# Optimization experiments

Measured on AMD Instinct MI355X. Metric: run time of the kernel, lower is better.

Reference implementation:

```python
import jax, jax.numpy as jnp
import numpy as np

B, S, H, W = 16, 512, 768, 8


def _enumerate_spans(S, W):
    # same enumeration order as the torch triple loop: for i, for j in [i, min(i+W, S)-1]
    starts, widths = [], []
    for i in range(S):
        for w in range(1, min(W, S - i) + 1):
            starts.append(i)
            widths.append(w)
    return np.asarray(starts, np.int32), np.asarray(widths, np.int32)


def setup_inputs() -> dict:
    key = jax.random.key(0)
    k1, k2, k3 = jax.random.split(key, 3)
    embeddings = jax.random.normal(k1, (B, S, H), dtype=jnp.float32)
    w_lin = jax.random.normal(k2, (2 * H + 1, H), dtype=jnp.float32) * 0.02
    b_lin = jax.random.normal(k3, (H,), dtype=jnp.float32) * 0.02
    starts, widths = _enumerate_spans(S, W)
    return {
        "embeddings": embeddings,
        "w_lin": w_lin,
        "b_lin": b_lin,
        "span_starts": jnp.asarray(starts),
        "span_widths": jnp.asarray(widths),
    }


def reference(embeddings, w_lin, b_lin, span_starts, span_widths):
    Bb, Ss, Hh = embeddings.shape
    cls_emb = embeddings[:, 0, :]  # [B, H]

    # Sliding-window running max: pooled[k, b, i, :] = max(embeddings[b, i:i+k+1, :])
    neg = jnp.full((Bb, W - 1, Hh), -jnp.inf, embeddings.dtype)
    padded = jnp.concatenate([embeddings, neg], axis=1)  # [B, S+W-1, H]
    cm = embeddings
    pools = [cm]
    for k in range(1, W):
        cm = jnp.maximum(cm, padded[:, k:k + Ss, :])
        pools.append(cm)
    pooled = jnp.stack(pools, axis=0)  # [W, B, S, H]

    # Gather each span's max-pooled embedding: [N, B, H] -> [B, N, H]
    span_max = pooled[span_widths - 1, :, span_starts, :]
    span_max = jnp.transpose(span_max, (1, 0, 2))

    N = span_starts.shape[0]
    cls_b = jnp.broadcast_to(cls_emb[:, None, :], (Bb, N, Hh))
    width_f = jnp.broadcast_to(
        span_widths.astype(embeddings.dtype)[None, :, None], (Bb, N, 1))
    feats = jnp.concatenate([span_max, cls_b, width_f], axis=-1)  # [B, N, 2H+1]

    span_reps = jnp.einsum("bnf,fh->bnh", feats, w_lin) + b_lin
    token_inputs = cls_emb  # [B, H]
    return token_inputs, span_reps.reshape(Bb * N, Hh)
```

## Files before the change

### kernel.cpp

```cpp
#include <hip/hip_runtime.h>
#include <hip/hip_bf16.h>
#include <stdint.h>

#define AS1 __attribute__((address_space(1)))
#define AS3 __attribute__((address_space(3)))

typedef float  f32x4  __attribute__((ext_vector_type(4)));
typedef __bf16 bf16x8 __attribute__((ext_vector_type(8)));
typedef __bf16 bf16x4 __attribute__((ext_vector_type(4)));
typedef short  s16x8  __attribute__((ext_vector_type(8)));

static constexpr int Bc = 16, Sc = 512, Hc = 768, NSPAN = 4068;

__global__ __launch_bounds__(256)
void prep_w1t(const float* __restrict__ w_lin, unsigned short* __restrict__ w1t, int swz) {
  __shared__ __align__(16) unsigned short T[64][80];
  int bidk = blockIdx.x % 12, bidn = blockIdx.x / 12;
  int k0 = bidk * 64, n0 = bidn * 64;
  int tid = threadIdx.x;
#pragma unroll
  for (int p = 0; p < 16; ++p) {
    int idx = p * 256 + tid;
    int kl = idx >> 6, nl = idx & 63;
    float v = w_lin[(size_t)(k0 + kl) * Hc + (n0 + nl)];
    __bf16 bv = (__bf16)v;
    T[nl][kl] = __builtin_bit_cast(unsigned short, bv);
  }
  __syncthreads();
#pragma unroll
  for (int qq = 0; qq < 2; ++qq) {
    int q = qq * 256 + tid;
    int nl = q >> 3, cc = q & 7;
    int n = n0 + nl;
    s16x8 v = *(const s16x8*)(&T[nl][cc * 8]);
    size_t off;
    if (swz) {
      int q8 = (k0 >> 3) + cc;
      off = (size_t)n * 1536 + (size_t)(q8 >> 2) * 64 + (size_t)((q8 & 3) ^ (n & 3)) * 16;
    } else {
      off = (size_t)n * 1536 + (size_t)k0 * 2 + (size_t)cc * 16;
    }
    *(s16x8*)((char*)w1t + off) = v;
  }
}

__global__ __launch_bounds__(256)
void cls_proj_kernel(const float* __restrict__ emb, const float* __restrict__ w_lin,
                     const float* __restrict__ b_lin, float* __restrict__ out,
                     float* __restrict__ cls_proj) {
  __shared__ float cls_s[Hc];
  int b = blockIdx.x / 3, hc = blockIdx.x % 3;
  int tid = threadIdx.x;
  const float* cls = emb + (size_t)b * Sc * Hc;
  for (int i = tid; i < Hc; i += 256) cls_s[i] = cls[i];
  __syncthreads();
  int h = hc * 256 + tid;
  const float* wp = w_lin + (size_t)Hc * Hc + h;
  float p0 = 0, p1 = 0, p2 = 0, p3 = 0, p4 = 0, p5 = 0, p6 = 0, p7 = 0;
  for (int f = 0; f < Hc; f += 8) {
    p0 += cls_s[f + 0] * wp[(size_t)(f + 0) * Hc];
    p1 += cls_s[f + 1] * wp[(size_t)(f + 1) * Hc];
    p2 += cls_s[f + 2] * wp[(size_t)(f + 2) * Hc];
    p3 += cls_s[f + 3] * wp[(size_t)(f + 3) * Hc];
    p4 += cls_s[f + 4] * wp[(size_t)(f + 4) * Hc];
    p5 += cls_s[f + 5] * wp[(size_t)(f + 5) * Hc];
    p6 += cls_s[f + 6] * wp[(size_t)(f + 6) * Hc];
    p7 += cls_s[f + 7] * wp[(size_t)(f + 7) * Hc];
  }
  float acc = b_lin[h] + (((p0 + p1) + (p2 + p3)) + ((p4 + p5) + (p6 + p7)));
  cls_proj[b * Hc + h] = acc;
  out[b * Hc + h] = cls_s[h];
}

__global__ __launch_bounds__(256)
void build_a(const float* __restrict__ emb, unsigned short* __restrict__ a_ws) {
  int blk = blockIdx.x;
  int b = blk >> 6, sb = blk & 63;
  int tid = threadIdx.x;
  int si = tid >> 5, kc = tid & 31;
  int s = (sb << 3) + si;
  const char* embB = (const char*)(emb + (size_t)b * Sc * Hc);
  uint32_t roff[8];
#pragma unroll
  for (int t = 0; t < 8; ++t) {
    int r = s + t;
    if (r > 511) r = 511;
    roff[t] = (uint32_t)r * (Hc * 4);
  }
  char* obase = (char*)a_ws + (size_t)((b * 512 + s) * 8) * 1536;
#pragma unroll
  for (int j = 0; j < 3; ++j) {
    int q8 = kc + (j << 5);
    uint32_t srcoff = (uint32_t)q8 * 32;
    f32x4 c0, c1;
#pragma unroll
    for (int t = 0; t < 8; ++t) {
      f32x4 a0 = *(const f32x4*)(embB + roff[t] + srcoff);
      f32x4 a1 = *(const f32x4*)(embB + roff[t] + srcoff + 16);
      if (t == 0) { c0 = a0; c1 = a1; }
      else {
        c0[0] = fmaxf(c0[0], a0[0]); c0[1] = fmaxf(c0[1], a0[1]);
        c0[2] = fmaxf(c0[2], a0[2]); c0[3] = fmaxf(c0[3], a0[3]);
        c1[0] = fmaxf(c1[0], a1[0]); c1[1] = fmaxf(c1[1], a1[1]);
        c1[2] = fmaxf(c1[2], a1[2]); c1[3] = fmaxf(c1[3], a1[3]);
      }
      bf16x8 p;
      p[0] = (__bf16)c0[0]; p[1] = (__bf16)c0[1]; p[2] = (__bf16)c0[2]; p[3] = (__bf16)c0[3];
      p[4] = (__bf16)c1[0]; p[5] = (__bf16)c1[1]; p[6] = (__bf16)c1[2]; p[7] = (__bf16)c1[3];
      size_t doff = (size_t)t * 1536 + (size_t)(q8 >> 2) * 64 + (size_t)((q8 & 3) ^ (t & 3)) * 16;
      *(bf16x8*)(obase + doff) = p;
    }
  }
}

__global__ __launch_bounds__(512, 1)
void gemm_pipe(const unsigned short* __restrict__ a_ws, const unsigned short* __restrict__ w1t,
               const float* __restrict__ cls_proj, const float* __restrict__ w_lin,
               float* __restrict__ out) {
  extern __shared__ __align__(16) char ldsb[];

  int wg = blockIdx.x;
  int wgid = (wg & 7) * 96 + (wg >> 3);
  int tile_n = wgid % 3, tile_m = wgid / 3;
  int b = tile_m >> 4;
  int n0 = tile_n << 8;
  int tid = threadIdx.x;
  int wid = tid >> 6, lane = tid & 63;
  int wave_m = wid >> 2, wave_n = wid & 3;
  int lq = lane >> 4, lr = lane & 15;

  const char* aw = (const char*)a_ws + ((size_t)tile_m << 8) * 1536;
  const char* bw = (const char*)w1t + (size_t)n0 * 1536;
  int srow = tid >> 2, schunk = tid & 3;

  const float* w2p = w_lin + (size_t)(2 * Hc) * Hc;
  float cp[4], w2[4];
#pragma unroll
  for (int ni = 0; ni < 4; ++ni) {
    int h = n0 + (wave_n << 6) + (ni << 4) + lr;
    cp[ni] = cls_proj[b * Hc + h];
    w2[ni] = w2p[h];
  }

  f32x4 acc[8][4];
  f32x4 zer = {0.f, 0.f, 0.f, 0.f};
#pragma unroll
  for (int i = 0; i < 8; ++i)
#pragma unroll
    for (int j = 0; j < 4; ++j) acc[i][j] = zer;

  bf16x8 bfr[4];

#define SB __builtin_amdgcn_sched_barrier(0)

#define STAGE_A(kt) {                                                          \
    const char* s_ = aw + (size_t)srow * 1536 + (size_t)(kt) * 64 + (schunk << 4); \
    char* d_ = ldsb + (((kt) & 3) << 15) + (tid << 4);                         \
    __builtin_amdgcn_global_load_lds((const AS1 uint32_t*)s_, (AS3 uint32_t*)d_, 16, 0, 0); \
    __builtin_amdgcn_global_load_lds((const AS1 uint32_t*)(s_ + 128 * 1536), (AS3 uint32_t*)(d_ + 8192), 16, 0, 0); }

#define STAGE_B(kt) {                                                          \
    const char* s_ = bw + (size_t)srow * 1536 + (size_t)(kt) * 64 + (schunk << 4); \
    char* d_ = ldsb + (((kt) & 3) << 15) + 16384 + (tid << 4);                 \
    __builtin_amdgcn_global_load_lds((const AS1 uint32_t*)s_, (AS3 uint32_t*)d_, 16, 0, 0); \
    __builtin_amdgcn_global_load_lds((const AS1 uint32_t*)(s_ + 128 * 1536), (AS3 uint32_t*)(d_ + 8192), 16, 0, 0); }

#define PH0(kt, DOSTAGE) {                                                     \
    const char* Ab_ = ldsb + (((kt) & 3) << 15);                               \
    const char* Bb_ = Ab_ + 16384;                                             \
    _Pragma("unroll") for (int ni = 0; ni < 4; ++ni) {                         \
      int n = (wave_n << 6) + (ni << 4) + lr;                                  \
      bfr[ni] = *(const bf16x8*)(Bb_ + n * 64 + ((lq ^ (n & 3)) << 4));        \
    }                                                                          \
    bf16x8 af[4];                                                              \
    _Pragma("unroll") for (int mi = 0; mi < 4; ++mi) {                         \
      int m = (wave_m << 7) + (mi << 4) + lr;                                  \
      af[mi] = *(const bf16x8*)(Ab_ + m * 64 + ((lq ^ (m & 3)) << 4));         \
    }                                                                          \
    if (DOSTAGE) { STAGE_A((kt) + 3); }                                        \
    SB; __builtin_amdgcn_s_barrier(); SB;                                      \
    __builtin_amdgcn_s_setprio(1);                                             \
    _Pragma("unroll") for (int mi = 0; mi < 4; ++mi)                           \
      _Pragma("unroll") for (int ni = 0; ni < 4; ++ni)                         \
        acc[mi][ni] = __builtin_amdgcn_mfma_f32_16x16x32_bf16(af[mi], bfr[ni], acc[mi][ni], 0, 0, 0); \
    __builtin_amdgcn_s_setprio(0);                                             \
    __builtin_amdgcn_s_barrier(); }

#define PH1(kt, DOSTAGE, WAITASM) {                                            \
    const char* Ab_ = ldsb + (((kt) & 3) << 15);                               \
    bf16x8 af[4];                                                              \
    _Pragma("unroll") for (int mi = 0; mi < 4; ++mi) {                         \
      int m = (wave_m << 7) + 64 + (mi << 4) + lr;                             \
      af[mi] = *(const bf16x8*)(Ab_ + m * 64 + ((lq ^ (m & 3)) << 4));         \
    }                                                                          \
    if (DOSTAGE) { STAGE_B((kt) + 3); }                                        \
    SB; __builtin_amdgcn_s_barrier(); SB;                                      \
    __builtin_amdgcn_s_setprio(1);                                             \
    _Pragma("unroll") for (int mi = 0; mi < 4; ++mi)                           \
      _Pragma("unroll") for (int ni = 0; ni < 4; ++ni)                         \
        acc[4 + mi][ni] = __builtin_amdgcn_mfma_f32_16x16x32_bf16(af[mi], bfr[ni], acc[4 + mi][ni], 0, 0, 0); \
    __builtin_amdgcn_s_setprio(0);                                             \
    SB; asm volatile(WAITASM ::: "memory"); SB;                                \
    __builtin_amdgcn_s_barrier(); }

  STAGE_A(-3 + 3); STAGE_B(0);
  STAGE_A(1 - 3 + 3);
  {
    const char* s_ = aw + (size_t)srow * 1536 + (size_t)1 * 64 + (schunk << 4);
    char* d_ = ldsb + ((1 & 3) << 15) + (tid << 4);
    __builtin_amdgcn_global_load_lds((const AS1 uint32_t*)s_, (AS3 uint32_t*)d_, 16, 0, 0);
    __builtin_amdgcn_global_load_lds((const AS1 uint32_t*)(s_ + 128 * 1536), (AS3 uint32_t*)(d_ + 8192), 16, 0, 0);
  }
  STAGE_B(1);
  {
    const char* s_ = aw + (size_t)srow * 1536 + (size_t)2 * 64 + (schunk << 4);
    char* d_ = ldsb + ((2 & 3) << 15) + (tid << 4);
    __builtin_amdgcn_global_load_lds((const AS1 uint32_t*)s_, (AS3 uint32_t*)d_, 16, 0, 0);
    __builtin_amdgcn_global_load_lds((const AS1 uint32_t*)(s_ + 128 * 1536), (AS3 uint32_t*)(d_ + 8192), 16, 0, 0);
  }
  STAGE_B(2);
  SB; asm volatile("s_waitcnt vmcnt(8)" ::: "memory"); SB;
  __builtin_amdgcn_s_barrier(); SB;

  for (int kt = 0; kt < 21; ++kt) {
    PH0(kt, 1);
    PH1(kt, 1, "s_waitcnt vmcnt(8)");
  }
  PH0(21, 0); PH1(21, 0, "s_waitcnt vmcnt(4)");
  PH0(22, 0); PH1(22, 0, "s_waitcnt vmcnt(0)");
  PH0(23, 0); PH1(23, 0, "s_nop 0");

  float* outp = out + Bc * Hc;
  int swb = (tile_m & 15) << 8;
  int hbase = n0 + (wave_n << 6) + lr;
#pragma unroll
  for (int mi = 0; mi < 8; ++mi) {
#pragma unroll
    for (int j = 0; j < 4; ++j) {
      int m = (wave_m << 7) + (mi << 4) + (lq << 2) + j;
      int sw = swb + m;
      int s = sw >> 3, w = (sw & 7) + 1;
      if (s + w <= 512) {
        int nsp = (s <= 504) ? sw
                             : (NSPAN - (((512 - s) * (513 - s)) >> 1) + w - 1);
        float* rowp = outp + ((size_t)b * NSPAN + nsp) * Hc + hbase;
        float wf = (float)w;
#pragma unroll
        for (int ni = 0; ni < 4; ++ni)
          rowp[ni << 4] = acc[mi][ni][j] + cp[ni] + wf * w2[ni];
      }
    }
  }
}

__global__ __launch_bounds__(512, 2)
void span_gemm_fused(const float* __restrict__ emb, const unsigned short* __restrict__ w1t,
                     const float* __restrict__ cls_proj, const float* __restrict__ w_lin,
                     float* __restrict__ out) {
  __shared__ __align__(16) unsigned short Ald[2][256 * 64];
  int wg = blockIdx.x;
  int wgid = (wg & 7) * 96 + (wg >> 3);
  int tile_n = wgid % 3, tile_m = wgid / 3;
  int b = tile_m >> 4;
  int s0 = (tile_m & 15) << 5;
  int n0 = tile_n << 8;
  int tid = threadIdx.x;
  int wid = tid >> 6, lane = tid & 63;
  int wave_m = wid >> 2, wave_n = wid & 3;
  int lq = lane >> 4, lr = lane & 15;
  const char* embC = (const char*)(emb + (size_t)b * Sc * Hc);
  int bi = tid >> 4, bkq = tid & 15;
  uint32_t rowoff[8];
#pragma unroll
  for (int t = 0; t < 8; ++t) {
    int r = s0 + bi + t;
    if (r > 511) r = 511;
    rowoff[t] = (uint32_t)r * (Hc * 4) + bkq * 16;
  }
  int awbase = (bi << 10) + ((bkq & 1) << 3);
  const unsigned short* bb = w1t + (size_t)(n0 + (wave_n << 6) + lr) * Hc + (lq << 3);
  f32x4 acc[8][4];
  f32x4 zer = {0.f, 0.f, 0.f, 0.f};
#pragma unroll
  for (int i = 0; i < 8; ++i)
#pragma unroll
    for (int j = 0; j < 4; ++j) acc[i][j] = zer;
  f32x4 rv[8];
  f32x4 cm;
  bf16x8 bfrA[4], bfrB[4];
#define FLOAD_RV(koff) _Pragma("unroll") for (int t = 0; t < 8; ++t) rv[t] = *(const f32x4*)(embC + rowoff[t] + (koff));
#define FLOAD_BFR(dst, koff) _Pragma("unroll") for (int ni = 0; ni < 4; ++ni) dst[ni] = *(const bf16x8*)(const void*)(bb + (size_t)ni * 16 * Hc + (koff));
#define FBUILD_T(an, t) { \
    if ((t) == 0) cm = rv[0]; \
    else { cm[0] = fmaxf(cm[0], rv[t][0]); cm[1] = fmaxf(cm[1], rv[t][1]); cm[2] = fmaxf(cm[2], rv[t][2]); cm[3] = fmaxf(cm[3], rv[t][3]); } \
    bf16x4 p; p[0] = (__bf16)cm[0]; p[1] = (__bf16)cm[1]; p[2] = (__bf16)cm[2]; p[3] = (__bf16)cm[3]; \
    int off = awbase + ((t) << 7) + (((bkq >> 1) ^ (t)) << 4); \
    *(uint2*)((an) + off) = __builtin_bit_cast(uint2, p); }
#define FQUAD(ab, mh, kk, bfr) { \
    bf16x8 af[4]; int cf = ((kk) << 2) + lq; \
    _Pragma("unroll") for (int mi = 0; mi < 4; ++mi) { \
      int m = (wave_m << 7) + ((((mh) << 2) + mi) << 4) + lr; \
      af[mi] = *(const bf16x8*)((ab) + (m << 7) + ((cf ^ (m & 7)) << 4)); } \
    __builtin_amdgcn_s_setprio(1); \
    _Pragma("unroll") for (int mi = 0; mi < 4; ++mi) \
      _Pragma("unroll") for (int ni = 0; ni < 4; ++ni) \
        acc[((mh) << 2) + mi][ni] = __builtin_amdgcn_mfma_f32_16x16x32_bf16(af[mi], bfr[ni], acc[((mh) << 2) + mi][ni], 0, 0, 0); \
    __builtin_amdgcn_s_setprio(0); }
  FLOAD_RV(0);
  {
    char* an0 = (char*)Ald[0];
#pragma unroll
    for (int t = 0; t < 8; ++t) FBUILD_T(an0, t);
  }
  FLOAD_BFR(bfrA, 0);
  FLOAD_RV(256);
  asm volatile("s_waitcnt lgkmcnt(0)" ::: "memory");
  __builtin_amdgcn_sched_barrier(0);
  __builtin_amdgcn_s_barrier();
  for (int kt = 0; kt < 12; ++kt) {
    int cur = kt & 1, nb = cur ^ 1;
    const char* ab = (const char*)Ald[cur];
    char* an = (char*)Ald[nb];
    FLOAD_BFR(bfrB, kt * 64 + 32);
    FQUAD(ab, 0, 0, bfrA);
    __builtin_amdgcn_sched_barrier(0);
    FQUAD(ab, 1, 0, bfrA);
    __builtin_amdgcn_sched_barrier(0);
    if (kt + 1 < 12) {
      FLOAD_BFR(bfrA, (kt + 1) * 64);
#pragma unroll
      for (int t = 0; t < 4; ++t) FBUILD_T(an, t);
    }
    FQUAD(ab, 0, 1, bfrB);
    __builtin_amdgcn_sched_barrier(0);
    if (kt + 1 < 12) {
#pragma unroll
      for (int t = 4; t < 8; ++t) FBUILD_T(an, t);
    }
    if (kt + 2 < 12) FLOAD_RV((kt + 2) * 256);
    FQUAD(ab, 1, 1, bfrB);
    if (kt + 1 < 12) {
      asm volatile("s_waitcnt lgkmcnt(0)" ::: "memory");
      __builtin_amdgcn_sched_barrier(0);
      __builtin_amdgcn_s_barrier();
      __builtin_amdgcn_sched_barrier(0);
    }
  }
  const float* w2p = w_lin + (size_t)(2 * Hc) * Hc;
  float* outp = out + Bc * Hc;
  int swb = (tile_m & 15) << 8;
  float cp[4], w2[4];
#pragma unroll
  for (int ni = 0; ni < 4; ++ni) {
    int h = n0 + (wave_n << 6) + (ni << 4) + lr;
    cp[ni] = cls_proj[b * Hc + h];
    w2[ni] = w2p[h];
  }
  int hbase = n0 + (wave_n << 6) + lr;
#pragma unroll
  for (int mi = 0; mi < 8; ++mi) {
#pragma unroll
    for (int j = 0; j < 4; ++j) {
      int m = (wave_m << 7) + (mi << 4) + (lq << 2) + j;
      int sw = swb + m;
      int s = sw >> 3, w = (sw & 7) + 1;
      if (s + w <= 512) {
        int nsp = (s <= 504) ? sw : (NSPAN - (((512 - s) * (513 - s)) >> 1) + w - 1);
        float* rowp = outp + ((size_t)b * NSPAN + nsp) * Hc + hbase;
        float wf = (float)w;
#pragma unroll
        for (int ni = 0; ni < 4; ++ni)
          rowp[ni << 4] = acc[mi][ni][j] + cp[ni] + wf * w2[ni];
      }
    }
  }
}

extern "C" void kernel_launch(void* const* d_in, const int* in_sizes, int n_in,
                              void* d_out, int out_size, void* d_ws, size_t ws_size,
                              hipStream_t stream) {
  const float* emb = (const float*)d_in[0];
  const float* w_lin = (const float*)d_in[1];
  const float* b_lin = (const float*)d_in[2];
  unsigned short* w1t = (unsigned short*)d_ws;
  float* cls_proj = (float*)((char*)d_ws + 1179648);
  unsigned short* a_ws = (unsigned short*)((char*)d_ws + 1228800);
  float* out = (float*)d_out;

  size_t need = 1228800ull + 100663296ull;
  if (ws_size >= need) {
    hipLaunchKernelGGL(prep_w1t, dim3(144), dim3(256), 0, stream, w_lin, w1t, 1);
    hipLaunchKernelGGL(cls_proj_kernel, dim3(48), dim3(256), 0, stream, emb, w_lin, b_lin, out, cls_proj);
    hipLaunchKernelGGL(build_a, dim3(1024), dim3(256), 0, stream, emb, a_ws);
    static int attr_set = 0;
    if (!attr_set) {
      hipFuncSetAttribute((const void*)gemm_pipe, hipFuncAttributeMaxDynamicSharedMemorySize, 131072);
      attr_set = 1;
    }
    hipLaunchKernelGGL(gemm_pipe, dim3(768), dim3(512), 131072, stream, a_ws, w1t, cls_proj, w_lin, out);
  } else {
    hipLaunchKernelGGL(prep_w1t, dim3(144), dim3(256), 0, stream, w_lin, w1t, 0);
    hipLaunchKernelGGL(cls_proj_kernel, dim3(48), dim3(256), 0, stream, emb, w_lin, b_lin, out, cls_proj);
    hipLaunchKernelGGL(span_gemm_fused, dim3(768), dim3(512), 0, stream, emb, w1t, cls_proj, w_lin, out);
  }
}
```

Baseline: 153.8 us.

## Re-tile A and W workspaces into k-major chunk tiles for contiguous staging

The bf16 A workspace and the transposed weights are re-laid out so that each 16-byte k-chunk of a 256-row tile sits contiguously, with k-chunks at a 4 KB stride. The GEMM's global-to-LDS staging then moves contiguous 1 KB blocks per wave, and its LDS fragment reads become plain linear offsets with no XOR swizzle. build_a is rewritten so each thread produces one (start, width) row and loops over k, writing fully coalesced 4 KB rows. The cost is that build_a's input reads are less coalesced: lanes read 32-byte pieces from different rows, branch on width, and run as fewer, longer blocks.

```diff
diff --git a/kernel.cpp b/kernel.cpp
--- a/kernel.cpp
+++ b/kernel.cpp
@@ -14,7 +14,7 @@
 
 __global__ __launch_bounds__(256)
 void prep_w1t(const float* __restrict__ w_lin, unsigned short* __restrict__ w1t, int swz) {
-  __shared__ __align__(16) unsigned short T[64][80];
+  __shared__ __align__(16) unsigned short T[64][88];
   int bidk = blockIdx.x % 12, bidn = blockIdx.x / 12;
   int k0 = bidk * 64, n0 = bidn * 64;
   int tid = threadIdx.x;
@@ -30,13 +30,13 @@
 #pragma unroll
   for (int qq = 0; qq < 2; ++qq) {
     int q = qq * 256 + tid;
-    int nl = q >> 3, cc = q & 7;
+    int cc = q >> 6, nl = q & 63;
     int n = n0 + nl;
     s16x8 v = *(const s16x8*)(&T[nl][cc * 8]);
     size_t off;
     if (swz) {
       int q8 = (k0 >> 3) + cc;
-      off = (size_t)n * 1536 + (size_t)(q8 >> 2) * 64 + (size_t)((q8 & 3) ^ (n & 3)) * 16;
+      off = (size_t)(n >> 8) * 393216 + (size_t)q8 * 4096 + (size_t)(n & 255) * 16;
     } else {
       off = (size_t)n * 1536 + (size_t)k0 * 2 + (size_t)cc * 16;
     }
@@ -75,41 +75,39 @@
 __global__ __launch_bounds__(256)
 void build_a(const float* __restrict__ emb, unsigned short* __restrict__ a_ws) {
   int blk = blockIdx.x;
-  int b = blk >> 6, sb = blk & 63;
-  int tid = threadIdx.x;
-  int si = tid >> 5, kc = tid & 31;
-  int s = (sb << 3) + si;
+  int b = blk >> 4;
+  int sbase = (blk & 15) << 5;
+  int tid = threadIdx.x;
+  int t = tid & 7;
+  int s = sbase + (tid >> 3);
   const char* embB = (const char*)(emb + (size_t)b * Sc * Hc);
-  uint32_t roff[8];
-#pragma unroll
-  for (int t = 0; t < 8; ++t) {
-    int r = s + t;
+  uint32_t ra[8];
+#pragma unroll
+  for (int tt = 0; tt < 8; ++tt) {
+    int r = s + tt;
     if (r > 511) r = 511;
-    roff[t] = (uint32_t)r * (Hc * 4);
-  }
-  char* obase = (char*)a_ws + (size_t)((b * 512 + s) * 8) * 1536;
-#pragma unroll
-  for (int j = 0; j < 3; ++j) {
-    int q8 = kc + (j << 5);
-    uint32_t srcoff = (uint32_t)q8 * 32;
-    f32x4 c0, c1;
-#pragma unroll
-    for (int t = 0; t < 8; ++t) {
-      f32x4 a0 = *(const f32x4*)(embB + roff[t] + srcoff);
-      f32x4 a1 = *(const f32x4*)(embB + roff[t] + srcoff + 16);
-      if (t == 0) { c0 = a0; c1 = a1; }
-      else {
+    ra[tt] = (uint32_t)r * (Hc * 4);
+  }
+  char* dst0 = (char*)a_ws + (size_t)blk * 393216 + (size_t)tid * 16;
+  for (int q8 = 0; q8 < 96; ++q8) {
+    uint32_t co = (uint32_t)q8 * 32;
+    f32x4 c0 = *(const f32x4*)(embB + ra[0] + co);
+    f32x4 c1 = *(const f32x4*)(embB + ra[0] + co + 16);
+#pragma unroll
+    for (int tt = 1; tt < 8; ++tt) {
+      if (tt <= t) {
+        f32x4 a0 = *(const f32x4*)(embB + ra[tt] + co);
+        f32x4 a1 = *(const f32x4*)(embB + ra[tt] + co + 16);
         c0[0] = fmaxf(c0[0], a0[0]); c0[1] = fmaxf(c0[1], a0[1]);
         c0[2] = fmaxf(c0[2], a0[2]); c0[3] = fmaxf(c0[3], a0[3]);
         c1[0] = fmaxf(c1[0], a1[0]); c1[1] = fmaxf(c1[1], a1[1]);
         c1[2] = fmaxf(c1[2], a1[2]); c1[3] = fmaxf(c1[3], a1[3]);
       }
-      bf16x8 p;
-      p[0] = (__bf16)c0[0]; p[1] = (__bf16)c0[1]; p[2] = (__bf16)c0[2]; p[3] = (__bf16)c0[3];
-      p[4] = (__bf16)c1[0]; p[5] = (__bf16)c1[1]; p[6] = (__bf16)c1[2]; p[7] = (__bf16)c1[3];
-      size_t doff = (size_t)t * 1536 + (size_t)(q8 >> 2) * 64 + (size_t)((q8 & 3) ^ (t & 3)) * 16;
-      *(bf16x8*)(obase + doff) = p;
-    }
+    }
+    bf16x8 p;
+    p[0] = (__bf16)c0[0]; p[1] = (__bf16)c0[1]; p[2] = (__bf16)c0[2]; p[3] = (__bf16)c0[3];
+    p[4] = (__bf16)c1[0]; p[5] = (__bf16)c1[1]; p[6] = (__bf16)c1[2]; p[7] = (__bf16)c1[3];
+    *(bf16x8*)(dst0 + (size_t)q8 * 4096) = p;
   }
 }
 
@@ -129,9 +127,10 @@
   int wave_m = wid >> 2, wave_n = wid & 3;
   int lq = lane >> 4, lr = lane & 15;
 
-  const char* aw = (const char*)a_ws + ((size_t)tile_m << 8) * 1536;
-  const char* bw = (const char*)w1t + (size_t)n0 * 1536;
-  int srow = tid >> 2, schunk = tid & 3;
+  const char* aw = (const char*)a_ws + (size_t)tile_m * 393216;
+  const char* bw = (const char*)w1t + (size_t)tile_n * 393216;
+  int u0 = wid << 1;
+  int lane16 = lane << 4;
 
   const float* w2p = w_lin + (size_t)(2 * Hc) * Hc;
   float cp[4], w2[4];
@@ -153,31 +152,27 @@
 
 #define SB __builtin_amdgcn_sched_barrier(0)
 
-#define STAGE_A(kt) {                                                          \
-    const char* s_ = aw + (size_t)srow * 1536 + (size_t)(kt) * 64 + (schunk << 4); \
-    char* d_ = ldsb + (((kt) & 3) << 15) + (tid << 4);                         \
-    __builtin_amdgcn_global_load_lds((const AS1 uint32_t*)s_, (AS3 uint32_t*)d_, 16, 0, 0); \
-    __builtin_amdgcn_global_load_lds((const AS1 uint32_t*)(s_ + 128 * 1536), (AS3 uint32_t*)(d_ + 8192), 16, 0, 0); }
-
-#define STAGE_B(kt) {                                                          \
-    const char* s_ = bw + (size_t)srow * 1536 + (size_t)(kt) * 64 + (schunk << 4); \
-    char* d_ = ldsb + (((kt) & 3) << 15) + 16384 + (tid << 4);                 \
-    __builtin_amdgcn_global_load_lds((const AS1 uint32_t*)s_, (AS3 uint32_t*)d_, 16, 0, 0); \
-    __builtin_amdgcn_global_load_lds((const AS1 uint32_t*)(s_ + 128 * 1536), (AS3 uint32_t*)(d_ + 8192), 16, 0, 0); }
+#define STAGE(kt, srcb, ldsoff) {                                              \
+    _Pragma("unroll") for (int g = 0; g < 2; ++g) {                            \
+      int u = u0 + g;                                                          \
+      const char* s_ = (srcb) + (size_t)((((kt) << 2) + (u >> 2)) << 12) + ((u & 3) << 10) + lane16; \
+      char* d_ = ldsb + (((kt) & 3) << 15) + (ldsoff) + (u << 10) + lane16;    \
+      __builtin_amdgcn_global_load_lds((const AS1 uint32_t*)s_, (AS3 uint32_t*)d_, 16, 0, 0); \
+    } }
 
 #define PH0(kt, DOSTAGE) {                                                     \
     const char* Ab_ = ldsb + (((kt) & 3) << 15);                               \
     const char* Bb_ = Ab_ + 16384;                                             \
     _Pragma("unroll") for (int ni = 0; ni < 4; ++ni) {                         \
       int n = (wave_n << 6) + (ni << 4) + lr;                                  \
-      bfr[ni] = *(const bf16x8*)(Bb_ + n * 64 + ((lq ^ (n & 3)) << 4));        \
+      bfr[ni] = *(const bf16x8*)(Bb_ + (lq << 12) + (n << 4));                 \
     }                                                                          \
     bf16x8 af[4];                                                              \
     _Pragma("unroll") for (int mi = 0; mi < 4; ++mi) {                         \
       int m = (wave_m << 7) + (mi << 4) + lr;                                  \
-      af[mi] = *(const bf16x8*)(Ab_ + m * 64 + ((lq ^ (m & 3)) << 4));         \
+      af[mi] = *(const bf16x8*)(Ab_ + (lq << 12) + (m << 4));                  \
     }                                                                          \
-    if (DOSTAGE) { STAGE_A((kt) + 3); }                                        \
+    if (DOSTAGE) STAGE((kt) + 3, aw, 0);                                       \
     SB; __builtin_amdgcn_s_barrier(); SB;                                      \
     __builtin_amdgcn_s_setprio(1);                                             \
     _Pragma("unroll") for (int mi = 0; mi < 4; ++mi)                           \
@@ -191,9 +186,9 @@
     bf16x8 af[4];                                                              \
     _Pragma("unroll") for (int mi = 0; mi < 4; ++mi) {                         \
       int m = (wave_m << 7) + 64 + (mi << 4) + lr;                             \
-      af[mi] = *(const bf16x8*)(Ab_ + m * 64 + ((lq ^ (m & 3)) << 4));         \
+      af[mi] = *(const bf16x8*)(Ab_ + (lq << 12) + (m << 4));                  \
     }                                                                          \
-    if (DOSTAGE) { STAGE_B((kt) + 3); }                                        \
+    if (DOSTAGE) STAGE((kt) + 3, bw, 16384);                                   \
     SB; __builtin_amdgcn_s_barrier(); SB;                                      \
     __builtin_amdgcn_s_setprio(1);                                             \
     _Pragma("unroll") for (int mi = 0; mi < 4; ++mi)                           \
@@ -203,22 +198,9 @@
     SB; asm volatile(WAITASM ::: "memory"); SB;                                \
     __builtin_amdgcn_s_barrier(); }
 
-  STAGE_A(-3 + 3); STAGE_B(0);
-  STAGE_A(1 - 3 + 3);
-  {
-    const char* s_ = aw + (size_t)srow * 1536 + (size_t)1 * 64 + (schunk << 4);
-    char* d_ = ldsb + ((1 & 3) << 15) + (tid << 4);
-    __builtin_amdgcn_global_load_lds((const AS1 uint32_t*)s_, (AS3 uint32_t*)d_, 16, 0, 0);
-    __builtin_amdgcn_global_load_lds((const AS1 uint32_t*)(s_ + 128 * 1536), (AS3 uint32_t*)(d_ + 8192), 16, 0, 0);
-  }
-  STAGE_B(1);
-  {
-    const char* s_ = aw + (size_t)srow * 1536 + (size_t)2 * 64 + (schunk << 4);
-    char* d_ = ldsb + ((2 & 3) << 15) + (tid << 4);
-    __builtin_amdgcn_global_load_lds((const AS1 uint32_t*)s_, (AS3 uint32_t*)d_, 16, 0, 0);
-    __builtin_amdgcn_global_load_lds((const AS1 uint32_t*)(s_ + 128 * 1536), (AS3 uint32_t*)(d_ + 8192), 16, 0, 0);
-  }
-  STAGE_B(2);
+  STAGE(0, aw, 0); STAGE(0, bw, 16384);
+  STAGE(1, aw, 0); STAGE(1, bw, 16384);
+  STAGE(2, aw, 0); STAGE(2, bw, 16384);
   SB; asm volatile("s_waitcnt vmcnt(8)" ::: "memory"); SB;
   __builtin_amdgcn_s_barrier(); SB;
 
@@ -391,7 +373,7 @@
   if (ws_size >= need) {
     hipLaunchKernelGGL(prep_w1t, dim3(144), dim3(256), 0, stream, w_lin, w1t, 1);
     hipLaunchKernelGGL(cls_proj_kernel, dim3(48), dim3(256), 0, stream, emb, w_lin, b_lin, out, cls_proj);
-    hipLaunchKernelGGL(build_a, dim3(1024), dim3(256), 0, stream, emb, a_ws);
+    hipLaunchKernelGGL(build_a, dim3(256), dim3(256), 0, stream, emb, a_ws);
     static int attr_set = 0;
     if (!attr_set) {
       hipFuncSetAttribute((const void*)gemm_pipe, hipFuncAttributeMaxDynamicSharedMemorySize, 131072);
```

After: 320.5 us. 2.08x slower.
